# Performance work log

Hardware: AMD Instinct MI355X
Metric: run time of the kernel (lower is better)

The kernel has to match this reference:

```python
import jax, jax.numpy as jnp
import numpy as np

EPS = 1e-5

def layer_norm(x, gamma, beta):
    # biased variance (unbiased=False), matching torch code
    mean = jnp.mean(x, axis=-1, keepdims=True)
    var = jnp.mean((x - mean) ** 2, axis=-1, keepdims=True)
    return (x - mean) / jnp.sqrt(var + EPS) * gamma + beta

def setup_inputs() -> dict:
    key = jax.random.key(0)
    ks = jax.random.split(key, 8)
    B, T, C, H = 2, 2048, 768, 12
    Dff = 4 * C
    s = lambda n: 1.0 / np.sqrt(n)
    return {
        "x": jax.random.normal(ks[0], (B, T, C), dtype=jnp.float32),
        "mask": jnp.ones((B, T), dtype=jnp.int32),
        "Wqkv": jax.random.normal(ks[1], (C, 3 * C), dtype=jnp.float32) * s(C),
        "bqkv": jnp.zeros((3 * C,), dtype=jnp.float32),
        "Wp": jax.random.normal(ks[2], (C, C), dtype=jnp.float32) * s(C),
        "bp": jnp.zeros((C,), dtype=jnp.float32),
        "gamma1": jnp.ones((1, 1, C), dtype=jnp.float32),
        "beta1": jnp.zeros((1, 1, C), dtype=jnp.float32),
        "W1": jax.random.normal(ks[3], (C, Dff), dtype=jnp.float32) * s(C),
        "b1": jnp.zeros((Dff,), dtype=jnp.float32),
        "W2": jax.random.normal(ks[4], (Dff, C), dtype=jnp.float32) * s(Dff),
        "b2": jnp.zeros((C,), dtype=jnp.float32),
        "gamma2": jnp.ones((1, 1, C), dtype=jnp.float32),
        "beta2": jnp.zeros((1, 1, C), dtype=jnp.float32),
    }

def reference(x, mask, Wqkv, bqkv, Wp, bp, gamma1, beta1, W1, b1, W2, b2, gamma2, beta2):
    B, T, C = x.shape
    H = 12
    D = C // H
    # --- multi-head attention (hand-rolled QK^T-softmax-V) ---
    qkv = x @ Wqkv + bqkv                                  # (B,T,3C)
    q, k, v = jnp.split(qkv, 3, axis=-1)
    q = q.reshape(B, T, H, D).transpose(0, 2, 1, 3)        # (B,H,T,D)
    k = k.reshape(B, T, H, D).transpose(0, 2, 1, 3)
    v = v.reshape(B, T, H, D).transpose(0, 2, 1, 3)
    scores = jnp.einsum('bhtd,bhsd->bhts', q, k) * (D ** -0.5)  # (B,H,T,T)
    pad = (mask == 0)[:, None, None, :]                    # (B,1,1,T)
    scores = jnp.where(pad, -jnp.inf, scores)
    weights = jax.nn.softmax(scores, axis=-1)
    attn = jnp.einsum('bhts,bhsd->bhtd', weights, v)       # (B,H,T,D)
    attn = attn.transpose(0, 2, 1, 3).reshape(B, T, C)
    attn = attn @ Wp + bp
    # --- post-sublayer LN then residual (as in source) ---
    out = x + layer_norm(attn, gamma1, beta1)
    # --- MLP with exact GELU ---
    h = jax.nn.gelu(out @ W1 + b1, approximate=False)
    mlp = h @ W2 + b2
    out = out + layer_norm(mlp, gamma2, beta2)
    return out
```

## Files before the change

### kernel.cpp

```cpp
#include <hip/hip_runtime.h>
#include <math.h>

#define BB 2
#define TT 2048
#define CC 768
#define NH 12
#define HD 64
#define DFF 3072
#define MM (BB*TT)

typedef _Float16 f16;
typedef unsigned long long u64;
typedef unsigned int u32;
typedef __attribute__((ext_vector_type(8))) _Float16 f16x8;
typedef __attribute__((ext_vector_type(4))) _Float16 f16x4;
typedef __attribute__((ext_vector_type(4))) float f32x4;

#define GLD_LDS(gptr, lptr) \
  __builtin_amdgcn_global_load_lds((const __attribute__((address_space(1))) void*)(gptr), \
                                   (__attribute__((address_space(3))) void*)(lptr), 16, 0, 0)

#if __has_builtin(__builtin_amdgcn_exp2f)
#define EXP2(x) __builtin_amdgcn_exp2f(x)
#else
#define EXP2(x) exp2f(x)
#endif

__global__ __launch_bounds__(256)
void convert_f16(const float* __restrict__ in, f16* __restrict__ out, int n4)
{
    const int i = blockIdx.x * 256 + threadIdx.x;
    if (i >= n4) return;
    float4 v = ((const float4*)in)[i];
    f16x4 o = {(f16)v.x, (f16)v.y, (f16)v.z, (f16)v.w};
    ((f16x4*)out)[i] = o;
}

__global__ __launch_bounds__(256)
void convert_transpose(const float* __restrict__ W, f16* __restrict__ Wt,
                       int K, int N)
{
    __shared__ float tile[32][33];
    const int k0 = blockIdx.x * 32, n0 = blockIdx.y * 32;
    const int r  = threadIdx.x >> 3;
    const int c4 = (threadIdx.x & 7) * 4;
    float4 v = *(const float4*)&W[(size_t)(k0 + r) * N + n0 + c4];
    tile[r][c4 + 0] = v.x; tile[r][c4 + 1] = v.y;
    tile[r][c4 + 2] = v.z; tile[r][c4 + 3] = v.w;
    __syncthreads();
    f16x4 o = {(f16)tile[c4 + 0][r], (f16)tile[c4 + 1][r],
               (f16)tile[c4 + 2][r], (f16)tile[c4 + 3][r]};
    *(f16x4*)&Wt[(size_t)(n0 + r) * K + k0 + c4] = o;
}

__global__ __launch_bounds__(64)
void build_maskbits(const int* __restrict__ mask, u64* __restrict__ mb)
{
    u64 bits = __ballot(mask[blockIdx.x * 64 + threadIdx.x] != 0);
    if (threadIdx.x == 0) mb[blockIdx.x] = bits;
}

template<int TM, int OUT_MODE, int GELU>
__global__ __launch_bounds__(256)
void gemm_mfma(const f16* __restrict__ A, const f16* __restrict__ Bt,
               const float* __restrict__ bias, void* __restrict__ Cout,
               f16* __restrict__ Vout, const int* __restrict__ maskp,
               int M, int N, int K)
{
    constexpr int NT = (TM == 128) ? 4 : 2;
    __shared__ f16 As[2][TM * 32];
    __shared__ f16 Bs[2][128 * 32];

    const int t = threadIdx.x;
    const int lane = t & 63, w = t >> 6;
    const int fr = lane & 15, quad = lane >> 4;
    const int row0 = blockIdx.y * TM, col0 = blockIdx.x * 128;
    const int wm = (TM == 128) ? (w & 1) * 64 : 0;
    const int wn = (TM == 128) ? (w >> 1) * 64 : w * 32;

    const int arow = w * (TM / 4) + (lane >> 2);
    const int brow = w * 32 + (lane >> 2);
    const int cg = (((lane & 3) ^ ((lane >> 3) & 3)) * 16);
    const char* ag = (const char*)(A  + (size_t)(row0 + arow) * K) + cg;
    const char* bg = (const char*)(Bt + (size_t)(col0 + brow) * K) + cg;
    const size_t rowK = (size_t)K * 2;
    const int wA = w * (TM / 4) * 32;
    const int wB = w * 32 * 32;

    const int sof = (quad ^ ((fr >> 1) & 3)) * 8;

    f32x4 acc[4][NT] = {};

    GLD_LDS(ag, &As[0][wA]);
    if (TM == 128) GLD_LDS(ag + 16 * rowK, &As[0][wA + 16 * 32]);
    GLD_LDS(bg, &Bs[0][wB]);
    GLD_LDS(bg + 16 * rowK, &Bs[0][wB + 16 * 32]);

    for (int k0 = 0; k0 < K; k0 += 32) {
        const int buf = (k0 >> 5) & 1;
        __syncthreads();
        if (k0 + 32 < K) {
            const size_t kb = (size_t)(k0 + 32) * 2;
            GLD_LDS(ag + kb, &As[buf ^ 1][wA]);
            if (TM == 128) GLD_LDS(ag + kb + 16 * rowK, &As[buf ^ 1][wA + 16 * 32]);
            GLD_LDS(bg + kb, &Bs[buf ^ 1][wB]);
            GLD_LDS(bg + kb + 16 * rowK, &Bs[buf ^ 1][wB + 16 * 32]);
        }
        f16x8 af[4], bf[NT];
#pragma unroll
        for (int mt = 0; mt < 4; ++mt)
            af[mt] = *(const f16x8*)&As[buf][(wm + mt * 16 + fr) * 32 + sof];
#pragma unroll
        for (int nt = 0; nt < NT; ++nt)
            bf[nt] = *(const f16x8*)&Bs[buf][(wn + nt * 16 + fr) * 32 + sof];
#pragma unroll
        for (int mt = 0; mt < 4; ++mt)
#pragma unroll
            for (int nt = 0; nt < NT; ++nt)
                acc[mt][nt] = __builtin_amdgcn_mfma_f32_16x16x32_f16(
                    af[mt], bf[nt], acc[mt][nt], 0, 0, 0);
    }

    float bvs[NT];
#pragma unroll
    for (int nt = 0; nt < NT; ++nt)
        bvs[nt] = bias[col0 + wn + nt * 16 + fr];
#pragma unroll
    for (int mt = 0; mt < 4; ++mt) {
        const int rowb = row0 + wm + mt * 16 + quad * 4;
        float mv[4] = {1.f, 1.f, 1.f, 1.f};
        if (OUT_MODE == 2 && col0 >= 1536) {
            int4 mi = *(const int4*)&maskp[rowb];
            mv[0] = mi.x ? 1.f : 0.f; mv[1] = mi.y ? 1.f : 0.f;
            mv[2] = mi.z ? 1.f : 0.f; mv[3] = mi.w ? 1.f : 0.f;
        }
#pragma unroll
        for (int nt = 0; nt < NT; ++nt) {
            const int col = col0 + wn + nt * 16 + fr;
            if (OUT_MODE == 2) {
                if (col0 < 1536) {
#pragma unroll
                    for (int v = 0; v < 4; ++v)
                        ((f16*)Cout)[(size_t)(rowb + v) * 1536 + col] = (f16)(acc[mt][nt][v] + bvs[nt]);
                } else {
                    const int dg = col - 1536;
                    const int hh = dg >> 6, dd = dg & 63;
                    const int bq = rowb >> 11, s = rowb & 2047;
                    f16x4 pk = {(f16)((acc[mt][nt][0] + bvs[nt]) * mv[0]),
                                (f16)((acc[mt][nt][1] + bvs[nt]) * mv[1]),
                                (f16)((acc[mt][nt][2] + bvs[nt]) * mv[2]),
                                (f16)((acc[mt][nt][3] + bvs[nt]) * mv[3])};
                    *(f16x4*)&Vout[(size_t)((bq * NH + hh) * HD + dd) * TT + s] = pk;
                }
            } else {
#pragma unroll
                for (int v = 0; v < 4; ++v) {
                    float o = acc[mt][nt][v] + bvs[nt];
                    if (GELU) o = 0.5f * o * (1.f + erff(o * 0.70710678118654752f));
                    if (OUT_MODE == 1) ((f16*)Cout)[(size_t)(rowb + v) * N + col] = (f16)o;
                    else               ((float*)Cout)[(size_t)(rowb + v) * N + col] = o;
                }
            }
        }
    }
}

__global__ __launch_bounds__(256)
void attn_mfma(const f16* __restrict__ qkh, const f16* __restrict__ vth,
               const u64* __restrict__ maskbits, f16* __restrict__ out)
{
    __shared__ __align__(16) char smem[50432];
    f16* Qs    = (f16*)smem;
    f16* KsB[2]; KsB[0] = (f16*)(smem + 8192);  KsB[1] = (f16*)(smem + 16384);
    f16* VtB[2]; VtB[0] = (f16*)(smem + 24576); VtB[1] = (f16*)(smem + 32768);
    f16* Ps    = (f16*)(smem + 40960);
    float* lredp = (float*)(smem + 50176);
    float* Ored  = (float*)smem;

    const int qt = blockIdx.x, h = blockIdx.y, b = blockIdx.z;
    const int t = threadIdx.x, lane = t & 63, w = t >> 6;
    const int wq = w >> 1, ws = w & 1;
    const int fr = lane & 15, quad = lane >> 4;

    const int srow = lane >> 3;
    const int scg  = ((lane & 7) ^ (srow & 7)) * 16;

    const char* qg = (const char*)qkh
        + (size_t)(b * TT + qt * 64 + w * 16 + srow) * 3072 + h * 128 + scg;
    const char* kg = (const char*)qkh
        + (size_t)(b * TT + w * 16 + srow) * 3072 + 1536 + h * 128 + scg;
    const char* vg = (const char*)vth
        + (size_t)((b * NH + h) * HD + w * 16 + srow) * (TT * 2) + scg;

    GLD_LDS(qg,            Qs + (w * 16) * 64);
    GLD_LDS(qg + 8 * 3072, Qs + (w * 16 + 8) * 64);
    GLD_LDS(kg,            KsB[0] + (w * 16) * 64);
    GLD_LDS(kg + 8 * 3072, KsB[0] + (w * 16 + 8) * 64);
    GLD_LDS(vg,            VtB[0] + (w * 16) * 64);
    GLD_LDS(vg + 8 * 4096, VtB[0] + (w * 16 + 8) * 64);
    kg += 64 * 3072;
    vg += 128;
    __syncthreads();

    const int sw0 = ((0 * 4 + quad) ^ (fr & 7)) * 8;
    const int sw1 = ((1 * 4 + quad) ^ (fr & 7)) * 8;

    f16x8 qf[2][2];
#pragma unroll
    for (int nt = 0; nt < 2; ++nt) {
        qf[nt][0] = *(const f16x8*)&Qs[(wq * 32 + nt * 16 + fr) * 64 + sw0];
        qf[nt][1] = *(const f16x8*)&Qs[(wq * 32 + nt * 16 + fr) * 64 + sw1];
    }

    f32x4 oacc[2][4] = {};
    f32x4 lacc[2] = {};

    for (int it = 0; it < TT / 64; ++it) {
        const int buf = it & 1;
        if (it) __syncthreads();
        if (it != TT / 64 - 1) {
            GLD_LDS(kg,            KsB[buf ^ 1] + (w * 16) * 64);
            GLD_LDS(kg + 8 * 3072, KsB[buf ^ 1] + (w * 16 + 8) * 64);
            GLD_LDS(vg,            VtB[buf ^ 1] + (w * 16) * 64);
            GLD_LDS(vg + 8 * 4096, VtB[buf ^ 1] + (w * 16 + 8) * 64);
            kg += 64 * 3072;
            vg += 128;
        }
        const u64 mb = maskbits[b * (TT / 64) + it];
        const f16* Ks = KsB[buf];
        const f16* Vt = VtB[buf];

        f32x4 sacc[2][2] = {};
#pragma unroll
        for (int mt = 0; mt < 2; ++mt) {
            f16x8 kf0 = *(const f16x8*)&Ks[(ws * 32 + mt * 16 + fr) * 64 + sw0];
            f16x8 kf1 = *(const f16x8*)&Ks[(ws * 32 + mt * 16 + fr) * 64 + sw1];
#pragma unroll
            for (int nt = 0; nt < 2; ++nt) {
                sacc[mt][nt] = __builtin_amdgcn_mfma_f32_16x16x32_f16(
                    kf0, qf[nt][0], sacc[mt][nt], 0, 0, 0);
                sacc[mt][nt] = __builtin_amdgcn_mfma_f32_16x16x32_f16(
                    kf1, qf[nt][1], sacc[mt][nt], 0, 0, 0);
            }
        }

#pragma unroll
        for (int mt = 0; mt < 2; ++mt)
#pragma unroll
            for (int nt = 0; nt < 2; ++nt) {
                float p0 = EXP2(fmaf(sacc[mt][nt][0], 0.18033688f, -11.5415603f));
                float p1 = EXP2(fmaf(sacc[mt][nt][1], 0.18033688f, -11.5415603f));
                float p2 = EXP2(fmaf(sacc[mt][nt][2], 0.18033688f, -11.5415603f));
                float p3 = EXP2(fmaf(sacc[mt][nt][3], 0.18033688f, -11.5415603f));
                f16x4 pk = {(f16)p0, (f16)p1, (f16)p2, (f16)p3};
                *(f16x4*)&Ps[(wq * 32 + nt * 16 + fr) * 72 + ws * 32 + mt * 16 + quad * 4] = pk;
            }

        const u32 mbyte = (u32)(mb >> (ws * 32 + quad * 8)) & 0xffu;
        f16x8 mf;
#pragma unroll
        for (int j = 0; j < 8; ++j)
            mf[j] = ((mbyte >> j) & 1u) ? (f16)1.0f : (f16)0.0f;

        f16x8 pf[2];
#pragma unroll
        for (int mt = 0; mt < 2; ++mt)
            pf[mt] = *(const f16x8*)&Ps[(wq * 32 + mt * 16 + fr) * 72 + ws * 32 + quad * 8];
#pragma unroll
        for (int mt = 0; mt < 2; ++mt) {
            lacc[mt] = __builtin_amdgcn_mfma_f32_16x16x32_f16(pf[mt], mf, lacc[mt], 0, 0, 0);
#pragma unroll
            for (int nt = 0; nt < 4; ++nt) {
                f16x8 vf = *(const f16x8*)&Vt[(nt * 16 + fr) * 64 +
                                              (((ws * 4 + quad) ^ (fr & 7)) * 8)];
                oacc[mt][nt] = __builtin_amdgcn_mfma_f32_16x16x32_f16(
                    pf[mt], vf, oacc[mt][nt], 0, 0, 0);
            }
        }
    }

    if (ws == 1) {
#pragma unroll
        for (int mt = 0; mt < 2; ++mt) {
            const int q = wq * 32 + mt * 16 + quad * 4;
#pragma unroll
            for (int nt = 0; nt < 4; ++nt)
#pragma unroll
                for (int v = 0; v < 4; ++v)
                    Ored[(q + v) * 64 + nt * 16 + fr] = oacc[mt][nt][v];
            if (fr == 0)
#pragma unroll
                for (int v = 0; v < 4; ++v) lredp[q + v] = lacc[mt][v];
        }
    }
    __syncthreads();
    if (ws == 0) {
#pragma unroll
        for (int mt = 0; mt < 2; ++mt) {
            const int q0 = wq * 32 + mt * 16 + quad * 4;
            float linv[4];
#pragma unroll
            for (int v = 0; v < 4; ++v)
                linv[v] = 1.f / (lacc[mt][v] + lredp[q0 + v]);
#pragma unroll
            for (int nt = 0; nt < 4; ++nt)
#pragma unroll
                for (int v = 0; v < 4; ++v) {
                    float o = oacc[mt][nt][v] + Ored[(q0 + v) * 64 + nt * 16 + fr];
                    out[(size_t)(b * TT + qt * 64 + q0 + v) * CC + h * HD + nt * 16 + fr]
                        = (f16)(o * linv[v]);
                }
        }
    }
}

template<int WRITE_H>
__global__ __launch_bounds__(256)
void ln_residual(const float* __restrict__ res, const f16* __restrict__ y,
                 const float* __restrict__ gamma, const float* __restrict__ beta,
                 float* __restrict__ outp, f16* __restrict__ outh)
{
    const int row = blockIdx.x;
    const int t = threadIdx.x;
    const f16* yr = y + (size_t)row * CC;
    const float v0 = (float)yr[t], v1 = (float)yr[t + 256], v2 = (float)yr[t + 512];
    float s  = v0 + v1 + v2;
    float sq = v0 * v0 + v1 * v1 + v2 * v2;
#pragma unroll
    for (int off = 1; off < 64; off <<= 1) {
        s  += __shfl_xor(s, off);
        sq += __shfl_xor(sq, off);
    }
    __shared__ float red[8];
    if ((t & 63) == 0) { red[t >> 6] = s; red[4 + (t >> 6)] = sq; }
    __syncthreads();
    s  = red[0] + red[1] + red[2] + red[3];
    sq = red[4] + red[5] + red[6] + red[7];
    const float mean = s * (1.f / 768.f);
    const float var  = sq * (1.f / 768.f) - mean * mean;
    const float rstd = rsqrtf(var + 1e-5f);
    const float* rr = res + (size_t)row * CC;
    float* orow = outp + (size_t)row * CC;
    const float o0 = rr[t]       + (v0 - mean) * rstd * gamma[t]       + beta[t];
    const float o1 = rr[t + 256] + (v1 - mean) * rstd * gamma[t + 256] + beta[t + 256];
    const float o2 = rr[t + 512] + (v2 - mean) * rstd * gamma[t + 512] + beta[t + 512];
    orow[t] = o0; orow[t + 256] = o1; orow[t + 512] = o2;
    if (WRITE_H) {
        f16* hrow = outh + (size_t)row * CC;
        hrow[t] = (f16)o0; hrow[t + 256] = (f16)o1; hrow[t + 512] = (f16)o2;
    }
}

extern "C" void kernel_launch(void* const* d_in, const int* in_sizes, int n_in,
                              void* d_out, int out_size, void* d_ws, size_t ws_size,
                              hipStream_t stream)
{
    const float* x     = (const float*)d_in[0];
    const int*   mask  = (const int*)  d_in[1];
    const float* Wqkv  = (const float*)d_in[2];
    const float* bqkv  = (const float*)d_in[3];
    const float* Wp    = (const float*)d_in[4];
    const float* bp    = (const float*)d_in[5];
    const float* g1    = (const float*)d_in[6];
    const float* be1   = (const float*)d_in[7];
    const float* W1    = (const float*)d_in[8];
    const float* b1    = (const float*)d_in[9];
    const float* W2    = (const float*)d_in[10];
    const float* b2    = (const float*)d_in[11];
    const float* g2    = (const float*)d_in[12];
    const float* be2   = (const float*)d_in[13];
    float* outp = (float*)d_out;

    char* wsb = (char*)d_ws;
    f16*   xh     = (f16*)(wsb);
    f16*   Wqkvt  = (f16*)(wsb + 6291456);
    f16*   qkh    = (f16*)(wsb + 9830400);
    f16*   vth    = (f16*)(wsb + 22413312);
    f16*   attnh  = (f16*)(wsb + 28704768);
    f16*   Wpt    = (f16*)(wsb + 34996224);
    float* out1f  = (float*)(wsb + 36175872);
    f16*   W1t    = (f16*)(wsb + 48758784);
    f16*   W2t    = (f16*)(wsb + 53477376);
    u64*   maskb  = (u64*)(wsb + 58195968);
    f16*   out1h  = (f16*)(wsb + 58196480);
    f16*   projh  = (f16*)(wsb);
    f16*   hbuf   = (f16*)(wsb + 9830400);
    f16*   mlph   = (f16*)(wsb);

    const dim3 blk(256);

    convert_f16<<<dim3(MM * CC / 1024), blk, 0, stream>>>(x, xh, MM * CC / 4);
    convert_transpose<<<dim3(CC / 32, 3 * CC / 32), blk, 0, stream>>>(Wqkv, Wqkvt, CC, 3 * CC);
    convert_transpose<<<dim3(CC / 32, CC / 32), blk, 0, stream>>>(Wp, Wpt, CC, CC);
    convert_transpose<<<dim3(CC / 32, DFF / 32), blk, 0, stream>>>(W1, W1t, CC, DFF);
    convert_transpose<<<dim3(DFF / 32, CC / 32), blk, 0, stream>>>(W2, W2t, DFF, CC);
    build_maskbits<<<dim3(MM / 64), dim3(64), 0, stream>>>(mask, maskb);

    gemm_mfma<128, 2, 0><<<dim3(3 * CC / 128, MM / 128), blk, 0, stream>>>(
        xh, Wqkvt, bqkv, qkh, vth, mask, MM, 3 * CC, CC);
    attn_mfma<<<dim3(TT / 64, NH, BB), blk, 0, stream>>>(qkh, vth, maskb, attnh);
    gemm_mfma<64, 1, 0><<<dim3(CC / 128, MM / 64), blk, 0, stream>>>(
        attnh, Wpt, bp, projh, nullptr, nullptr, MM, CC, CC);
    ln_residual<1><<<dim3(MM), blk, 0, stream>>>(x, projh, g1, be1, out1f, out1h);
    gemm_mfma<128, 1, 1><<<dim3(DFF / 128, MM / 128), blk, 0, stream>>>(
        out1h, W1t, b1, hbuf, nullptr, nullptr, MM, DFF, CC);
    gemm_mfma<64, 1, 0><<<dim3(CC / 128, MM / 64), blk, 0, stream>>>(
        hbuf, W2t, b2, mlph, nullptr, nullptr, MM, CC, DFF);
    ln_residual<0><<<dim3(MM), blk, 0, stream>>>(out1f, mlph, g2, be2, outp, nullptr);
}
```

Baseline: 309.0 us.

## Remap GEMM and attention blocks per XCD and use a fast polynomial GELU

GEMM and attention launches now use a 1D grid. Block ids are remapped so that consecutive ids, which round-robin across the 8 XCDs, assign each XCD a contiguous band of rows, or for attention a set of (batch, head) pairs. This improves L2 reuse of A tiles and K/V within each XCD. The exact erff-based GELU is replaced by the Abramowitz-Stegun erf polynomial with a hardware reciprocal and exp2, cutting epilogue ALU cost. The approximation has error around 1e-7 relative to erf, and the mapping assumes the grid sizes divide evenly by the XCD grouping.

```diff
diff --git a/kernel.cpp b/kernel.cpp
--- a/kernel.cpp
+++ b/kernel.cpp
@@ -25,6 +25,26 @@
 #else
 #define EXP2(x) exp2f(x)
 #endif
+
+#if __has_builtin(__builtin_amdgcn_rcpf)
+#define RCP(x) __builtin_amdgcn_rcpf(x)
+#else
+#define RCP(x) (1.f / (x))
+#endif
+
+__device__ __forceinline__ float gelu_f(float x)
+{
+    const float y = fabsf(x) * 0.70710678118654752f;
+    const float t = RCP(fmaf(0.3275911f, y, 1.f));
+    float p = fmaf(1.061405429f, t, -1.453152027f);
+    p = fmaf(p, t, 1.421413741f);
+    p = fmaf(p, t, -0.284496736f);
+    p = fmaf(p, t, 0.254829592f);
+    p = p * t;
+    const float e = EXP2(-y * y * 1.4426950408889634f);
+    const float er = copysignf(1.f - p * e, x);
+    return 0.5f * x * (1.f + er);
+}
 
 __global__ __launch_bounds__(256)
 void convert_f16(const float* __restrict__ in, f16* __restrict__ out, int n4)
@@ -68,13 +88,19 @@
                int M, int N, int K)
 {
     constexpr int NT = (TM == 128) ? 4 : 2;
+    constexpr int G  = 512 / TM;
     __shared__ f16 As[2][TM * 32];
     __shared__ f16 Bs[2][128 * 32];
+
+    const int id = blockIdx.x;
+    const int xcd = id & 7, j = id >> 3;
+    const int by = xcd * G + (j & (G - 1));
+    const int bx = j / G;
 
     const int t = threadIdx.x;
     const int lane = t & 63, w = t >> 6;
     const int fr = lane & 15, quad = lane >> 4;
-    const int row0 = blockIdx.y * TM, col0 = blockIdx.x * 128;
+    const int row0 = by * TM, col0 = bx * 128;
     const int wm = (TM == 128) ? (w & 1) * 64 : 0;
     const int wn = (TM == 128) ? (w >> 1) * 64 : w * 32;
 
@@ -156,7 +182,7 @@
 #pragma unroll
                 for (int v = 0; v < 4; ++v) {
                     float o = acc[mt][nt][v] + bvs[nt];
-                    if (GELU) o = 0.5f * o * (1.f + erff(o * 0.70710678118654752f));
+                    if (GELU) o = gelu_f(o);
                     if (OUT_MODE == 1) ((f16*)Cout)[(size_t)(rowb + v) * N + col] = (f16)o;
                     else               ((float*)Cout)[(size_t)(rowb + v) * N + col] = o;
                 }
@@ -177,7 +203,12 @@
     float* lredp = (float*)(smem + 50176);
     float* Ored  = (float*)smem;
 
-    const int qt = blockIdx.x, h = blockIdx.y, b = blockIdx.z;
+    const int id = blockIdx.x;
+    const int xcd = id & 7, j = id >> 3;
+    const int pair = xcd * 3 + j % 3;
+    const int qt = j / 3;
+    const int b = pair / NH, h = pair % NH;
+
     const int t = threadIdx.x, lane = t & 63, w = t >> 6;
     const int wq = w >> 1, ws = w & 1;
     const int fr = lane & 15, quad = lane >> 4;
@@ -259,8 +290,8 @@
         const u32 mbyte = (u32)(mb >> (ws * 32 + quad * 8)) & 0xffu;
         f16x8 mf;
 #pragma unroll
-        for (int j = 0; j < 8; ++j)
-            mf[j] = ((mbyte >> j) & 1u) ? (f16)1.0f : (f16)0.0f;
+        for (int jj = 0; jj < 8; ++jj)
+            mf[jj] = ((mbyte >> jj) & 1u) ? (f16)1.0f : (f16)0.0f;
 
         f16x8 pf[2];
 #pragma unroll
@@ -396,15 +427,15 @@
     convert_transpose<<<dim3(DFF / 32, CC / 32), blk, 0, stream>>>(W2, W2t, DFF, CC);
     build_maskbits<<<dim3(MM / 64), dim3(64), 0, stream>>>(mask, maskb);
 
-    gemm_mfma<128, 2, 0><<<dim3(3 * CC / 128, MM / 128), blk, 0, stream>>>(
+    gemm_mfma<128, 2, 0><<<dim3((3 * CC / 128) * (MM / 128)), blk, 0, stream>>>(
         xh, Wqkvt, bqkv, qkh, vth, mask, MM, 3 * CC, CC);
-    attn_mfma<<<dim3(TT / 64, NH, BB), blk, 0, stream>>>(qkh, vth, maskb, attnh);
-    gemm_mfma<64, 1, 0><<<dim3(CC / 128, MM / 64), blk, 0, stream>>>(
+    attn_mfma<<<dim3((TT / 64) * NH * BB), blk, 0, stream>>>(qkh, vth, maskb, attnh);
+    gemm_mfma<64, 1, 0><<<dim3((CC / 128) * (MM / 64)), blk, 0, stream>>>(
         attnh, Wpt, bp, projh, nullptr, nullptr, MM, CC, CC);
     ln_residual<1><<<dim3(MM), blk, 0, stream>>>(x, projh, g1, be1, out1f, out1h);
-    gemm_mfma<128, 1, 1><<<dim3(DFF / 128, MM / 128), blk, 0, stream>>>(
+    gemm_mfma<128, 1, 1><<<dim3((DFF / 128) * (MM / 128)), blk, 0, stream>>>(
         out1h, W1t, b1, hbuf, nullptr, nullptr, MM, DFF, CC);
-    gemm_mfma<64, 1, 0><<<dim3(CC / 128, MM / 64), blk, 0, stream>>>(
+    gemm_mfma<64, 1, 0><<<dim3((CC / 128) * (MM / 64)), blk, 0, stream>>>(
         hbuf, W2t, b2, mlph, nullptr, nullptr, MM, CC, DFF);
     ln_residual<0><<<dim3(MM), blk, 0, stream>>>(out1f, mlph, g2, be2, outp, nullptr);
 }
```

After: 291.5 us. -5.7%, faster.
